# Performance work log

Measured on AMD Instinct MI355X. Metric: run time of the kernel, lower is better.

Reference implementation:

```python
import jax, jax.numpy as jnp
import numpy as np

V, D, F, B, E = 50257, 1024, 2048, 64, 512  # vocab, embed/rnn dim, fc hidden, batch, entities


def setup_inputs() -> dict:
    key = jax.random.key(0)
    ks = jax.random.split(key, 12)
    s = 0.05
    return {
        "entity_hiddens": jax.random.normal(ks[0], (B, E, D), jnp.float32),
        "question": jax.random.randint(ks[1], (B,), 0, V),
        "keys_mask": jax.random.randint(ks[2], (B, E), 0, 2).astype(bool),
        "emb": jax.random.normal(ks[3], (V, D), jnp.float32) * s,
        "W1": jax.random.normal(ks[4], (D, F), jnp.float32) * s,
        "b1": jnp.zeros((F,), jnp.float32),
        "W2": jax.random.normal(ks[5], (F, D), jnp.float32) * s,
        "b2": jnp.zeros((D,), jnp.float32),
        "A": jax.random.normal(ks[6], (D, D), jnp.float32) * s,  # entity_attn_matrix
        "H": jax.random.normal(ks[7], (D, D), jnp.float32) * s,
        "Ws": jax.random.normal(ks[8], (D, V), jnp.float32) * s,
        "bs": jnp.zeros((V,), jnp.float32),
    }


def reference(entity_hiddens, question, keys_mask, emb, W1, b1, W2, b2, A, H, Ws, bs):
    # embed question token and project: [B, D]
    eq0 = emb[question]
    q = jax.nn.relu(eq0 @ W1 + b1) @ W2 + b2
    # attention_entities actual returned math:
    # reduce_sum(expand_dims(q@A,1) * boolean_mask(entities, mask), axis=1)
    # == (q @ A) * sum over all masked entities (a single [D] vector)
    qA = q @ A  # [B, D]
    m = keys_mask.astype(entity_hiddens.dtype)
    ent_sum = jnp.sum(entity_hiddens * m[..., None], axis=(0, 1))  # [D]
    u = qA * ent_sum  # [B, D]
    logits = (q + u @ H) @ Ws + bs  # [B, V]
    return jax.nn.softmax(logits, axis=-1)
```

## Files before the change

### kernel.cpp

```cpp
#include <hip/hip_runtime.h>
#include <stdint.h>

#define V_ 50257
#define D_ 1024
#define F_ 2048
#define B_ 64
#define E_ 512
#define ROWS_ (B_*E_)

typedef __attribute__((ext_vector_type(8))) short bf16x8;
typedef __attribute__((ext_vector_type(4))) float f32x4;
typedef __attribute__((ext_vector_type(4), aligned(4))) float f32x4a;

__device__ __forceinline__ unsigned rne1(float a) {
  unsigned u = __float_as_uint(a);
  return (u + 0x7FFFu + ((u >> 16) & 1u)) >> 16;
}

__device__ __forceinline__ float waveMax(float v) {
#pragma unroll
  for (int o = 32; o > 0; o >>= 1) v = fmaxf(v, __shfl_xor(v, o, 64));
  return v;
}
__device__ __forceinline__ float waveSum(float v) {
#pragma unroll
  for (int o = 32; o > 0; o >>= 1) v += __shfl_xor(v, o, 64);
  return v;
}


__device__ __forceinline__ void ent_partial_body(int bid, const float* __restrict__ eh,
                                                 const void* __restrict__ mask,
                                                 float* __restrict__ part) {
  __shared__ int s_mode;
  const int tid = threadIdx.x;
  const uint32_t* mu = (const uint32_t*)mask;
  int f = 0;
  for (int i = tid; i < (ROWS_ / 4); i += 256) {
    uint32_t u = mu[i];
    if (u == 0x3F800000u) f |= 2;
    else if (u & 0xFFFFFF00u) f |= 1;
  }
  if (tid == 0) s_mode = 0;
  __syncthreads();
  if (f) atomicOr(&s_mode, f);
  __syncthreads();
  const int sm = s_mode;
  const int mode = (sm & 1) ? 1 : ((sm & 2) ? 2 : 0);

  float4 acc = make_float4(0.f, 0.f, 0.f, 0.f);
  const float4* eh4 = (const float4*)eh;
  for (int row = bid; row < ROWS_; row += 512) {
    bool on;
    if (mode == 1)      on = ((const unsigned char*)mask)[row] != 0;
    else if (mode == 2) on = ((const float*)mask)[row] != 0.f;
    else                on = ((const int*)mask)[row] != 0;
    if (on) {
      float4 v = eh4[(size_t)row * (D_ / 4) + tid];
      acc.x += v.x; acc.y += v.y; acc.z += v.z; acc.w += v.w;
    }
  }
  ((float4*)part)[(size_t)bid * (D_ / 4) + tid] = acc;
}

__device__ __forceinline__ void ent_reduce_body(int bid, const float* __restrict__ part,
                                                float* __restrict__ entsum) {
  int d = bid * 256 + threadIdx.x;
  float s0 = 0.f, s1 = 0.f, s2 = 0.f, s3 = 0.f;
#pragma unroll 8
  for (int i = 0; i < 512; i += 4) {
    s0 += part[(size_t)(i    ) * D_ + d];
    s1 += part[(size_t)(i + 1) * D_ + d];
    s2 += part[(size_t)(i + 2) * D_ + d];
    s3 += part[(size_t)(i + 3) * D_ + d];
  }
  entsum[d] = (s0 + s1) + (s2 + s3);
}

__device__ __forceinline__ void gemm64_body(int bx, int by, const float* __restrict__ X,
                                            const int* __restrict__ gatherIdx,
                                            const float* __restrict__ emb,
                                            const float* __restrict__ W,
                                            int K, int N, int KB, float* __restrict__ part) {
  const int l  = threadIdx.x & 63;
  const int rg = __builtin_amdgcn_readfirstlane((int)(threadIdx.x >> 6));
  const int c  = bx * 64 + l;
  const int k0 = by * KB;
  const int m0 = rg * 16;

  const float* Xp = gatherIdx ? emb : X;
  int rb[16];
#pragma unroll
  for (int r = 0; r < 16; ++r) {
    int m = m0 + r;
    rb[r] = gatherIdx ? gatherIdx[m] * K : m * K;
  }

  float acc[16];
#pragma unroll
  for (int r = 0; r < 16; ++r) acc[r] = 0.f;

  for (int k = k0; k < k0 + KB; k += 8) {
    float wv[8];
#pragma unroll
    for (int j = 0; j < 8; ++j) wv[j] = W[(size_t)(k + j) * N + c];
#pragma unroll
    for (int r = 0; r < 16; ++r) {
      float4 x0 = *(const float4*)&Xp[rb[r] + k];
      float4 x1 = *(const float4*)&Xp[rb[r] + k + 4];
      acc[r] = fmaf(x0.x, wv[0], acc[r]);
      acc[r] = fmaf(x0.y, wv[1], acc[r]);
      acc[r] = fmaf(x0.z, wv[2], acc[r]);
      acc[r] = fmaf(x0.w, wv[3], acc[r]);
      acc[r] = fmaf(x1.x, wv[4], acc[r]);
      acc[r] = fmaf(x1.y, wv[5], acc[r]);
      acc[r] = fmaf(x1.z, wv[6], acc[r]);
      acc[r] = fmaf(x1.w, wv[7], acc[r]);
    }
  }
  size_t base = (size_t)by * ((size_t)64 * N);
#pragma unroll
  for (int r = 0; r < 16; ++r) part[base + (size_t)(m0 + r) * N + c] = acc[r];
}

template<int NSPLIT>
__device__ __forceinline__ void reduce_body_t(int bid, const float* __restrict__ part,
                                              int MN, int N,
                                              const float* __restrict__ vecB,
                                              const float* __restrict__ addend,
                                              int mode, float* __restrict__ dst,
                                              unsigned short* __restrict__ ph,
                                              unsigned short* __restrict__ pl) {
  int idx = bid * 256 + threadIdx.x;
  if (idx >= MN) return;

  if (mode == 4) {
    const int d   = idx;
    const int j   = d & 7;
    const int l   = (d >> 3) & 63;
    const int m   = (d >> 9) & 3;
    const int tg  = d >> 11;
    const int col = l & 15;
    const int g   = l >> 4;
    const int row = m * 16 + col;
    const int kk  = tg * 32 + g * 8 + j;
    const int src = row * 1024 + kk;
    float s = 0.f;
#pragma unroll
    for (int i = 0; i < NSPLIT; ++i) s += part[(size_t)i * MN + src];
    s += addend[src];
    unsigned hi = rne1(s);
    float hif = __uint_as_float(hi << 16);
    ph[d] = (unsigned short)hi;
    pl[d] = (unsigned short)rne1(s - hif);
    return;
  }

  float s = 0.f;
#pragma unroll
  for (int i = 0; i < NSPLIT; ++i) s += part[(size_t)i * MN + idx];
  int c = idx & (N - 1);
  if (mode == 1)      { s += vecB[c]; s = s > 0.f ? s : 0.f; dst[idx] = s; }
  else if (mode == 2) { s += vecB[c]; dst[idx] = s; }
  else                { s *= vecB[c]; dst[idx] = s; }
}

__global__ void k_p1(const float* __restrict__ eh, const void* __restrict__ mask,
                     float* __restrict__ entpart, const int* __restrict__ ques,
                     const float* __restrict__ emb, const float* __restrict__ W1,
                     float* __restrict__ gpart) {
  int bid = blockIdx.x;
  if (bid < 512) ent_partial_body(bid, eh, mask, entpart);
  else {
    int b2 = bid - 512;
    gemm64_body(b2 & 31, b2 >> 5, nullptr, ques, emb, W1, 1024, 2048, 64, gpart);
  }
}

__global__ void k_p2(const float* __restrict__ entpart, float* __restrict__ entsum,
                     const float* __restrict__ gpart, const float* __restrict__ b1,
                     float* __restrict__ hbuf) {
  int bid = blockIdx.x;
  if (bid < 4) ent_reduce_body(bid, entpart, entsum);
  else reduce_body_t<16>(bid - 4, gpart, 64 * 2048, 2048, b1, nullptr, 1, hbuf, nullptr, nullptr);
}

__global__ void k_gemm64(const float* __restrict__ X, const float* __restrict__ W,
                         int K, int N, int KB, float* __restrict__ part) {
  gemm64_body(blockIdx.x, blockIdx.y, X, nullptr, nullptr, W, K, N, KB, part);
}

template<int NSPLIT>
__global__ void k_reduce_t(const float* __restrict__ part, int MN, int N,
                           const float* __restrict__ vecB, const float* __restrict__ addend,
                           int mode, float* __restrict__ dst,
                           unsigned short* __restrict__ ph, unsigned short* __restrict__ pl) {
  reduce_body_t<NSPLIT>(blockIdx.x, part, MN, N, vecB, addend, mode, dst, ph, pl);
}

__global__ __launch_bounds__(256, 2) void k_gemm_big(const unsigned short* __restrict__ zpkh,
                                                     const unsigned short* __restrict__ zpkl,
                                                     const float* __restrict__ Ws,
                                                     float* __restrict__ part2) {
  __shared__ float lds[2][32 * 260];
  const int t   = threadIdx.x;
  const int l   = t & 63;
  const int w   = t >> 6;
  const int col = l & 15;
  const int g   = l >> 4;
  const int c0  = (blockIdx.x < 196) ? blockIdx.x * 256 : (V_ - 256);
  const int kbase = blockIdx.y * 512;

  f32x4 acc[4][4];
#pragma unroll
  for (int n = 0; n < 4; ++n)
#pragma unroll
    for (int m = 0; m < 4; ++m) acc[n][m] = (f32x4){0.f, 0.f, 0.f, 0.f};

  {
    f32x4a gg[8];
#pragma unroll
    for (int i = 0; i < 8; ++i) {
      const int r = w + 4 * i;
      gg[i] = *(const f32x4a*)(Ws + (size_t)(kbase + r) * V_ + c0 + 4 * l);
    }
#pragma unroll
    for (int i = 0; i < 8; ++i) {
      const int r = w + 4 * i;
      *(f32x4*)&lds[0][r * 260 + 4 * l] = (f32x4)gg[i];
    }
  }
  __syncthreads();

  for (int tt = 0; tt < 16; ++tt) {
    const int buf = tt & 1;
    const int tg  = (kbase >> 5) + tt;

    bf16x8 ah[4], al[4];
#pragma unroll
    for (int m = 0; m < 4; ++m) {
      const int zb = ((tg * 4 + m) * 64 + l) * 8;
      ah[m] = *(const bf16x8*)(zpkh + zb);
      al[m] = *(const bf16x8*)(zpkl + zb);
    }

    f32x4a gg[8];
    if (tt + 1 < 16) {
      const float* wb = Ws + (size_t)(kbase + (tt + 1) * 32) * V_ + c0 + 4 * l;
#pragma unroll
      for (int i = 0; i < 8; ++i)
        gg[i] = *(const f32x4a*)(wb + (size_t)(w + 4 * i) * V_);
    }
    __builtin_amdgcn_sched_barrier(0);

#pragma unroll
    for (int n = 0; n < 4; ++n) {
      float f[8];
#pragma unroll
      for (int j = 0; j < 8; ++j)
        f[j] = lds[buf][(g * 8 + j) * 260 + w * 64 + n * 16 + col];

      union { bf16x8 v; unsigned u[4]; } bh, bl;
#pragma unroll
      for (int j = 0; j < 4; ++j) {
        unsigned h0 = rne1(f[2 * j]);
        unsigned h1 = rne1(f[2 * j + 1]);
        float h0f = __uint_as_float(h0 << 16);
        float h1f = __uint_as_float(h1 << 16);
        bh.u[j] = h0 | (h1 << 16);
        bl.u[j] = rne1(f[2 * j] - h0f) | (rne1(f[2 * j + 1] - h1f) << 16);
      }
#pragma unroll
      for (int m = 0; m < 4; ++m) acc[n][m] = __builtin_amdgcn_mfma_f32_16x16x32_bf16(ah[m], bh.v, acc[n][m], 0, 0, 0);
#pragma unroll
      for (int m = 0; m < 4; ++m) acc[n][m] = __builtin_amdgcn_mfma_f32_16x16x32_bf16(ah[m], bl.v, acc[n][m], 0, 0, 0);
#pragma unroll
      for (int m = 0; m < 4; ++m) acc[n][m] = __builtin_amdgcn_mfma_f32_16x16x32_bf16(al[m], bh.v, acc[n][m], 0, 0, 0);
    }
    __builtin_amdgcn_sched_barrier(0);

    if (tt + 1 < 16) {
#pragma unroll
      for (int i = 0; i < 8; ++i) {
        const int r = w + 4 * i;
        *(f32x4*)&lds[buf ^ 1][r * 260 + 4 * l] = (f32x4)gg[i];
      }
    }
    __syncthreads();
  }

  float* pout = part2 + (size_t)blockIdx.y * ((size_t)64 * V_);
#pragma unroll
  for (int n = 0; n < 4; ++n) {
    const int c = c0 + w * 64 + n * 16 + col;
#pragma unroll
    for (int m = 0; m < 4; ++m)
#pragma unroll
      for (int i = 0; i < 4; ++i)
        pout[(size_t)(m * 16 + g * 4 + i) * V_ + c] = acc[n][m][i];
  }
}

#define SM_CHUNK 12565

__global__ void k_softmax1(const float* __restrict__ part2, const float* __restrict__ bs,
                           float2* __restrict__ stats) {
  __shared__ float smx[4], ssum[4];
  const int r = blockIdx.x >> 2, q = blockIdx.x & 3;
  const int beg = q * SM_CHUNK;
  const int end = (beg + SM_CHUNK < V_) ? beg + SM_CHUNK : V_;
  const float* p0 = part2 + (size_t)r * V_;
  const float* p1 = part2 + (size_t)64 * V_ + (size_t)r * V_;

  float mx = -3.4e38f;
  for (int i = beg + threadIdx.x; i < end; i += 256) mx = fmaxf(mx, p0[i] + p1[i] + bs[i]);
  mx = waveMax(mx);
  if ((threadIdx.x & 63) == 0) smx[threadIdx.x >> 6] = mx;
  __syncthreads();
  mx = fmaxf(fmaxf(smx[0], smx[1]), fmaxf(smx[2], smx[3]));

  float s = 0.f;
  for (int i = beg + threadIdx.x; i < end; i += 256) s += __expf(p0[i] + p1[i] + bs[i] - mx);
  s = waveSum(s);
  if ((threadIdx.x & 63) == 0) ssum[threadIdx.x >> 6] = s;
  __syncthreads();
  s = (ssum[0] + ssum[1]) + (ssum[2] + ssum[3]);

  if (threadIdx.x == 0) stats[blockIdx.x] = make_float2(mx, s);
}

__global__ void k_softmax2(const float* __restrict__ part2, const float* __restrict__ bs,
                           const float2* __restrict__ stats, float* __restrict__ out) {
  const int r = blockIdx.x >> 2, q = blockIdx.x & 3;
  float2 s0 = stats[r * 4 + 0], s1 = stats[r * 4 + 1];
  float2 s2 = stats[r * 4 + 2], s3 = stats[r * 4 + 3];
  float M = fmaxf(fmaxf(s0.x, s1.x), fmaxf(s2.x, s3.x));
  float S = s0.y * __expf(s0.x - M) + s1.y * __expf(s1.x - M)
          + s2.y * __expf(s2.x - M) + s3.y * __expf(s3.x - M);
  float inv = 1.f / S;
  const int beg = q * SM_CHUNK;
  const int end = (beg + SM_CHUNK < V_) ? beg + SM_CHUNK : V_;
  const float* p0 = part2 + (size_t)r * V_;
  const float* p1 = part2 + (size_t)64 * V_ + (size_t)r * V_;
  float* orow = out + (size_t)r * V_;
  for (int i = beg + threadIdx.x; i < end; i += 256)
    orow[i] = __expf(p0[i] + p1[i] + bs[i] - M) * inv;
}

extern "C" void kernel_launch(void* const* d_in, const int* in_sizes, int n_in,
                              void* d_out, int out_size, void* d_ws, size_t ws_size,
                              hipStream_t stream) {
  const float* eh   = (const float*)d_in[0];
  const int*   ques = (const int*)d_in[1];
  const void*  mask = d_in[2];
  const float* emb  = (const float*)d_in[3];
  const float* W1   = (const float*)d_in[4];
  const float* b1   = (const float*)d_in[5];
  const float* W2   = (const float*)d_in[6];
  const float* b2   = (const float*)d_in[7];
  const float* A    = (const float*)d_in[8];
  const float* H    = (const float*)d_in[9];
  const float* Ws   = (const float*)d_in[10];
  const float* bs   = (const float*)d_in[11];
  float* out = (float*)d_out;
  char* ws = (char*)d_ws;

  float*          gpart   = (float*)(ws + 0);
  float*          entpart = (float*)(ws + 12866048);
  float*          entsum  = (float*)(ws + 14963200);
  float*          hbuf    = (float*)(ws + 14967296);
  float*          qbuf    = (float*)(ws + 15491584);
  float*          ubuf    = (float*)(ws + 15753728);
  unsigned short* zpkh    = (unsigned short*)(ws + 16015872);
  unsigned short* zpkl    = (unsigned short*)(ws + 16146944);
  float2*         stats   = (float2*)(ws + 16278016);
  float*          part2   = (float*)(ws + 20971520);

  k_p1<<<1024, 256, 0, stream>>>(eh, mask, entpart, ques, emb, W1, gpart);
  k_p2<<<516, 256, 0, stream>>>(entpart, entsum, gpart, b1, hbuf);

  k_gemm64<<<dim3(16, 32), 256, 0, stream>>>(hbuf, W2, 2048, 1024, 64, gpart);
  k_reduce_t<32><<<256, 256, 0, stream>>>(gpart, 64 * 1024, 1024, b2, nullptr, 2, qbuf, nullptr, nullptr);

  k_gemm64<<<dim3(16, 16), 256, 0, stream>>>(qbuf, A, 1024, 1024, 64, gpart);
  k_reduce_t<16><<<256, 256, 0, stream>>>(gpart, 64 * 1024, 1024, entsum, nullptr, 3, ubuf, nullptr, nullptr);

  k_gemm64<<<dim3(16, 16), 256, 0, stream>>>(ubuf, H, 1024, 1024, 64, gpart);
  k_reduce_t<16><<<256, 256, 0, stream>>>(gpart, 64 * 1024, 1024, nullptr, qbuf, 4, nullptr, zpkh, zpkl);

  k_gemm_big<<<dim3(197, 2), 256, 0, stream>>>(zpkh, zpkl, Ws, part2);

  k_softmax1<<<256, 256, 0, stream>>>(part2, bs, stats);
  k_softmax2<<<256, 256, 0, stream>>>(part2, bs, stats, out);

  (void)in_sizes; (void)n_in; (void)out_size; (void)ws_size;
}
```

Measured before the change: 251.7 us.

## Fuse small-GEMM chain into one cooperative kernel; swizzle LDS and use packed bf16 cvt

Replaces eight small launches (embedding/W1 GEMM, reductions, W2/A/H GEMMs) with one cooperative kernel of 512 blocks that separates the stages with grid.sync. It falls back to the old launches if the cooperative launch fails. In the big Ws GEMM it XOR-swizzles the LDS layout to cut bank conflicts and replaces the manual bf16 round-to-nearest with v_cvt_pk_bf16_f32. The point is to remove launch gaps and ALU work, at the cost of grid-wide barrier latency and fewer blocks for the first stage (512 instead of 1024).

```diff
diff --git a/kernel.cpp b/kernel.cpp
--- a/kernel.cpp
+++ b/kernel.cpp
@@ -1,5 +1,8 @@
 #include <hip/hip_runtime.h>
+#include <hip/hip_cooperative_groups.h>
 #include <stdint.h>
+
+namespace cg = cooperative_groups;
 
 #define V_ 50257
 #define D_ 1024
@@ -15,6 +18,12 @@
 __device__ __forceinline__ unsigned rne1(float a) {
   unsigned u = __float_as_uint(a);
   return (u + 0x7FFFu + ((u >> 16) & 1u)) >> 16;
+}
+
+__device__ __forceinline__ unsigned cvtpk(float a, float b) {
+  unsigned r;
+  asm("v_cvt_pk_bf16_f32 %0, %1, %2" : "=v"(r) : "v"(a), "v"(b));
+  return r;
 }
 
 __device__ __forceinline__ float waveMax(float v) {
@@ -165,6 +174,37 @@
   else                { s *= vecB[c]; dst[idx] = s; }
 }
 
+__global__ void k_chain(const float* __restrict__ eh, const void* __restrict__ mask,
+                        float* __restrict__ entpart, const int* __restrict__ ques,
+                        const float* __restrict__ emb, const float* __restrict__ W1,
+                        float* __restrict__ gpart, float* __restrict__ entsum,
+                        const float* __restrict__ b1, float* __restrict__ hbuf,
+                        const float* __restrict__ W2, const float* __restrict__ b2,
+                        float* __restrict__ qbuf, const float* __restrict__ A,
+                        float* __restrict__ ubuf, const float* __restrict__ H,
+                        unsigned short* __restrict__ zpkh, unsigned short* __restrict__ zpkl) {
+  cg::grid_group grid = cg::this_grid();
+  const int b = blockIdx.x;
+
+  ent_partial_body(b, eh, mask, entpart);
+  gemm64_body(b & 31, b >> 5, nullptr, ques, emb, W1, 1024, 2048, 64, gpart);
+  grid.sync();
+  reduce_body_t<16>(b, gpart, 64 * 2048, 2048, b1, nullptr, 1, hbuf, nullptr, nullptr);
+  if (b < 4) ent_reduce_body(b, entpart, entsum);
+  grid.sync();
+  gemm64_body(b & 15, b >> 4, hbuf, nullptr, nullptr, W2, 2048, 1024, 64, gpart);
+  grid.sync();
+  if (b < 256) reduce_body_t<32>(b, gpart, 64 * 1024, 1024, b2, nullptr, 2, qbuf, nullptr, nullptr);
+  grid.sync();
+  if (b < 256) gemm64_body(b & 15, b >> 4, qbuf, nullptr, nullptr, A, 1024, 1024, 64, gpart);
+  grid.sync();
+  if (b < 256) reduce_body_t<16>(b, gpart, 64 * 1024, 1024, entsum, nullptr, 3, ubuf, nullptr, nullptr);
+  grid.sync();
+  if (b < 256) gemm64_body(b & 15, b >> 4, ubuf, nullptr, nullptr, H, 1024, 1024, 64, gpart);
+  grid.sync();
+  if (b < 256) reduce_body_t<16>(b, gpart, 64 * 1024, 1024, nullptr, qbuf, 4, nullptr, zpkh, zpkl);
+}
+
 __global__ void k_p1(const float* __restrict__ eh, const void* __restrict__ mask,
                      float* __restrict__ entpart, const int* __restrict__ ques,
                      const float* __restrict__ emb, const float* __restrict__ W1,
@@ -210,6 +250,7 @@
   const int g   = l >> 4;
   const int c0  = (blockIdx.x < 196) ? blockIdx.x * 256 : (V_ - 256);
   const int kbase = blockIdx.y * 512;
+  const int xr  = (g & 1) << 4;
 
   f32x4 acc[4][4];
 #pragma unroll
@@ -227,7 +268,7 @@
 #pragma unroll
     for (int i = 0; i < 8; ++i) {
       const int r = w + 4 * i;
-      *(f32x4*)&lds[0][r * 260 + 4 * l] = (f32x4)gg[i];
+      *(f32x4*)&lds[0][r * 260 + ((4 * l) ^ (((r >> 3) & 1) << 4))] = (f32x4)gg[i];
     }
   }
   __syncthreads();
@@ -255,20 +296,20 @@
 
 #pragma unroll
     for (int n = 0; n < 4; ++n) {
+      const int cread = w * 64 + n * 16 + col;
       float f[8];
 #pragma unroll
       for (int j = 0; j < 8; ++j)
-        f[j] = lds[buf][(g * 8 + j) * 260 + w * 64 + n * 16 + col];
+        f[j] = lds[buf][(g * 8 + j) * 260 + (cread ^ xr)];
 
       union { bf16x8 v; unsigned u[4]; } bh, bl;
 #pragma unroll
       for (int j = 0; j < 4; ++j) {
-        unsigned h0 = rne1(f[2 * j]);
-        unsigned h1 = rne1(f[2 * j + 1]);
-        float h0f = __uint_as_float(h0 << 16);
-        float h1f = __uint_as_float(h1 << 16);
-        bh.u[j] = h0 | (h1 << 16);
-        bl.u[j] = rne1(f[2 * j] - h0f) | (rne1(f[2 * j + 1] - h1f) << 16);
+        unsigned h = cvtpk(f[2 * j], f[2 * j + 1]);
+        float h0f = __uint_as_float(h << 16);
+        float h1f = __uint_as_float(h & 0xFFFF0000u);
+        bh.u[j] = h;
+        bl.u[j] = cvtpk(f[2 * j] - h0f, f[2 * j + 1] - h1f);
       }
 #pragma unroll
       for (int m = 0; m < 4; ++m) acc[n][m] = __builtin_amdgcn_mfma_f32_16x16x32_bf16(ah[m], bh.v, acc[n][m], 0, 0, 0);
@@ -283,7 +324,7 @@
 #pragma unroll
       for (int i = 0; i < 8; ++i) {
         const int r = w + 4 * i;
-        *(f32x4*)&lds[buf ^ 1][r * 260 + 4 * l] = (f32x4)gg[i];
+        *(f32x4*)&lds[buf ^ 1][r * 260 + ((4 * l) ^ (((r >> 3) & 1) << 4))] = (f32x4)gg[i];
       }
     }
     __syncthreads();
@@ -376,17 +417,29 @@
   float2*         stats   = (float2*)(ws + 16278016);
   float*          part2   = (float*)(ws + 20971520);
 
-  k_p1<<<1024, 256, 0, stream>>>(eh, mask, entpart, ques, emb, W1, gpart);
-  k_p2<<<516, 256, 0, stream>>>(entpart, entsum, gpart, b1, hbuf);
-
-  k_gemm64<<<dim3(16, 32), 256, 0, stream>>>(hbuf, W2, 2048, 1024, 64, gpart);
-  k_reduce_t<32><<<256, 256, 0, stream>>>(gpart, 64 * 1024, 1024, b2, nullptr, 2, qbuf, nullptr, nullptr);
-
-  k_gemm64<<<dim3(16, 16), 256, 0, stream>>>(qbuf, A, 1024, 1024, 64, gpart);
-  k_reduce_t<16><<<256, 256, 0, stream>>>(gpart, 64 * 1024, 1024, entsum, nullptr, 3, ubuf, nullptr, nullptr);
-
-  k_gemm64<<<dim3(16, 16), 256, 0, stream>>>(ubuf, H, 1024, 1024, 64, gpart);
-  k_reduce_t<16><<<256, 256, 0, stream>>>(gpart, 64 * 1024, 1024, nullptr, qbuf, 4, nullptr, zpkh, zpkl);
+  {
+    const float* a_eh = eh; const void* a_mask = mask; float* a_entpart = entpart;
+    const int* a_ques = ques; const float* a_emb = emb; const float* a_W1 = W1;
+    float* a_gpart = gpart; float* a_entsum = entsum; const float* a_b1 = b1;
+    float* a_hbuf = hbuf; const float* a_W2 = W2; const float* a_b2 = b2;
+    float* a_qbuf = qbuf; const float* a_A = A; float* a_ubuf = ubuf;
+    const float* a_H = H; unsigned short* a_zpkh = zpkh; unsigned short* a_zpkl = zpkl;
+    void* args[] = {&a_eh, &a_mask, &a_entpart, &a_ques, &a_emb, &a_W1, &a_gpart,
+                    &a_entsum, &a_b1, &a_hbuf, &a_W2, &a_b2, &a_qbuf, &a_A, &a_ubuf,
+                    &a_H, &a_zpkh, &a_zpkl};
+    hipError_t ce = hipLaunchCooperativeKernel((void*)k_chain, dim3(512), dim3(256),
+                                               args, 0, stream);
+    if (ce != hipSuccess) {
+      k_p1<<<1024, 256, 0, stream>>>(eh, mask, entpart, ques, emb, W1, gpart);
+      k_p2<<<516, 256, 0, stream>>>(entpart, entsum, gpart, b1, hbuf);
+      k_gemm64<<<dim3(16, 32), 256, 0, stream>>>(hbuf, W2, 2048, 1024, 64, gpart);
+      k_reduce_t<32><<<256, 256, 0, stream>>>(gpart, 64 * 1024, 1024, b2, nullptr, 2, qbuf, nullptr, nullptr);
+      k_gemm64<<<dim3(16, 16), 256, 0, stream>>>(qbuf, A, 1024, 1024, 64, gpart);
+      k_reduce_t<16><<<256, 256, 0, stream>>>(gpart, 64 * 1024, 1024, entsum, nullptr, 3, ubuf, nullptr, nullptr);
+      k_gemm64<<<dim3(16, 16), 256, 0, stream>>>(ubuf, H, 1024, 1024, 64, gpart);
+      k_reduce_t<16><<<256, 256, 0, stream>>>(gpart, 64 * 1024, 1024, nullptr, qbuf, 4, nullptr, zpkh, zpkl);
+    }
+  }
 
   k_gemm_big<<<dim3(197, 2), 256, 0, stream>>>(zpkh, zpkl, Ws, part2);
 
```

Measured after the change: 681.0 us. +170.5%, slower.
